# Kernel tuning notes

Hardware: AMD Instinct MI355X
Metric: run time of the kernel (lower is better)

Reference implementation:

```python
import jax, jax.numpy as jnp
import numpy as np

B, N, DIM = 128, 577, 1024
HEADS, DIM_HEAD = 16, 64
INNER = HEADS * DIM_HEAD  # must equal DIM per module's reshape constraint


def setup_inputs() -> dict:
    key = jax.random.key(0)
    ks = jax.random.split(key, 6)
    x = jax.random.normal(ks[0], (B, N, DIM), jnp.float32)
    W_proj = jax.random.normal(ks[1], (INNER, DIM), jnp.float32) * (DIM ** -0.5)
    step_x = jax.random.normal(ks[2], (HEADS, 1, 1), jnp.float32)
    step_rep = jax.random.normal(ks[3], (HEADS, 1, 1), jnp.float32)
    W_out = jax.random.normal(ks[4], (DIM, INNER), jnp.float32) * (INNER ** -0.5)
    b_out = jnp.zeros((DIM,), jnp.float32)
    return {"x": x, "W_proj": W_proj, "step_x": step_x,
            "step_rep": step_rep, "W_out": W_out, "b_out": b_out}


def _attention(q, k, v, scale):
    # q: (b,h,q,d), k/v: (b,h,k,d)
    attn = jax.nn.softmax(jnp.einsum('bhqd,bhkd->bhqk', q, k) * scale, axis=-1)
    out = jnp.einsum('bhqk,bhkd->bhqd', attn, v)
    return out, attn


def reference(x, W_proj, step_x, step_rep, W_out, b_out):
    b, n, c = x.shape
    heads = step_x.shape[0]
    dim_head = W_proj.shape[0] // heads
    scale = dim_head ** -0.5
    h = int(n ** 0.5)          # grid side; n = h*h + 1 (cls token dropped for pooling)
    s = h // 8                 # adaptive pool block size (h divisible by 8)

    w = x @ W_proj.T  # (b, n, inner)

    # AdaptiveAvgPool2d((8,8)) on (b,c,h,h) == 3x3 block mean here; token order row-major
    rep = w[:, :-1, :].reshape(b, 8, s, 8, s, c).mean(axis=(2, 4))  # (b,8,8,c)
    rep = rep.reshape(b, 64, heads, dim_head).transpose(0, 2, 1, 3)  # (b,h,64,d)
    wq = w.reshape(b, n, heads, dim_head).transpose(0, 2, 1, 3)      # (b,h,n,d)

    rep_delta, attn = _attention(rep, wq, wq, scale)  # attn: (b,h,64,n)
    rep = rep + step_rep * rep_delta

    x_delta, _ = _attention(rep, rep, rep, scale)     # (b,h,64,d)
    # attn.T @ x_delta : (b,h,n,64) @ (b,h,64,d) -> (b,h,n,d)
    x_delta = jnp.einsum('bhkn,bhkd->bhnd', attn, x_delta)
    x_delta = step_x * x_delta
    x_delta = x_delta.transpose(0, 2, 1, 3).reshape(b, n, heads * dim_head)
    return x_delta @ W_out.T + b_out
```

## Files before the change

### kernel.cpp

```cpp
#include <hip/hip_runtime.h>
#include <hip/hip_bf16.h>

typedef __hip_bfloat16 bf16;
typedef __attribute__((ext_vector_type(8))) short short8;
typedef __attribute__((ext_vector_type(4))) float floatx4;

#define N_TOK 577
#define DIM_ 1024

__device__ __forceinline__ float bf2f(bf16 v) { return __bfloat162float(v); }
__device__ __forceinline__ bf16 f2bf(float v) { return __float2bfloat16(v); }
__device__ __forceinline__ short f2bf_s(float f) {
  unsigned u = __builtin_bit_cast(unsigned, f);
  u = (u + 0x7FFFu + ((u >> 16) & 1u)) >> 16;
  return (short)u;
}

#define GLL16(g, l) __builtin_amdgcn_global_load_lds( \
    (const __attribute__((address_space(1))) void*)(g), \
    (__attribute__((address_space(3))) void*)(l), 16, 0, 0)

template <typename T>
__device__ __forceinline__ short8 ldfrag(const T* base) {
  if constexpr (sizeof(T) == 2) {
    return *(const short8*)base;
  } else {
    const floatx4* p = (const floatx4*)base;
    floatx4 a = p[0], b = p[1];
    short8 o;
    o[0] = f2bf_s(a[0]); o[1] = f2bf_s(a[1]); o[2] = f2bf_s(a[2]); o[3] = f2bf_s(a[3]);
    o[4] = f2bf_s(b[0]); o[5] = f2bf_s(b[1]); o[6] = f2bf_s(b[2]); o[7] = f2bf_s(b[3]);
    return o;
  }
}

__global__ __launch_bounds__(256) void cvt_f32_bf16_kernel(
    const float* __restrict__ in, bf16* __restrict__ out, long n8)
{
  const long stride = (long)gridDim.x * 256;
  for (long i = (long)blockIdx.x * 256 + threadIdx.x; i < n8; i += stride) {
    const floatx4* p = (const floatx4*)in + i * 2;
    floatx4 a = p[0], b = p[1];
    short8 o;
    o[0] = f2bf_s(a[0]); o[1] = f2bf_s(a[1]); o[2] = f2bf_s(a[2]); o[3] = f2bf_s(a[3]);
    o[4] = f2bf_s(b[0]); o[5] = f2bf_s(b[1]); o[6] = f2bf_s(b[2]); o[7] = f2bf_s(b[3]);
    ((short8*)out)[i] = o;
  }
}

template <typename TA, typename TB, typename TC>
__global__ __launch_bounds__(256) void gemm_bt_kernel(
    const TA* __restrict__ A, const TB* __restrict__ Bw,
    const float* __restrict__ bias, TC* __restrict__ C,
    int M, int N, int K)
{
  __shared__ TA As[128 * 32];
  __shared__ TB Bs[128 * 32];
  const int tid = threadIdx.x;
  const int wave = tid >> 6, lane = tid & 63;
  const int r = lane & 15, q = lane >> 4;
  const int m0 = blockIdx.y * 128, n0 = blockIdx.x * 128;
  const int wm = (wave >> 1) * 64, wn = (wave & 1) * 64;

  floatx4 acc[4][4];
#pragma unroll
  for (int i = 0; i < 4; ++i)
#pragma unroll
    for (int j = 0; j < 4; ++j) acc[i][j] = (floatx4){0.f, 0.f, 0.f, 0.f};

  const TA* Ab = A + (size_t)m0 * K;
  const TB* Bb = Bw + (size_t)n0 * K;
  const int srowA2 = wave * 32 + (lane >> 2), skkA2 = (lane & 3) * 8;
  const int srowA4 = wave * 32 + (lane >> 3), skkA4 = (lane & 7) * 4;

  for (int k0 = 0; k0 < K; k0 += 32) {
    if constexpr (sizeof(TA) == 2) {
      GLL16(Ab + (size_t)srowA2 * K + k0 + skkA2, As + wave * 1024);
      GLL16(Ab + (size_t)(srowA2 + 16) * K + k0 + skkA2, As + wave * 1024 + 512);
    } else {
      GLL16(Ab + (size_t)srowA4 * K + k0 + skkA4, As + wave * 1024);
      GLL16(Ab + (size_t)(srowA4 + 8) * K + k0 + skkA4, As + wave * 1024 + 256);
      GLL16(Ab + (size_t)(srowA4 + 16) * K + k0 + skkA4, As + wave * 1024 + 512);
      GLL16(Ab + (size_t)(srowA4 + 24) * K + k0 + skkA4, As + wave * 1024 + 768);
    }
    if constexpr (sizeof(TB) == 2) {
      GLL16(Bb + (size_t)srowA2 * K + k0 + skkA2, Bs + wave * 1024);
      GLL16(Bb + (size_t)(srowA2 + 16) * K + k0 + skkA2, Bs + wave * 1024 + 512);
    } else {
      GLL16(Bb + (size_t)srowA4 * K + k0 + skkA4, Bs + wave * 1024);
      GLL16(Bb + (size_t)(srowA4 + 8) * K + k0 + skkA4, Bs + wave * 1024 + 256);
      GLL16(Bb + (size_t)(srowA4 + 16) * K + k0 + skkA4, Bs + wave * 1024 + 512);
      GLL16(Bb + (size_t)(srowA4 + 24) * K + k0 + skkA4, Bs + wave * 1024 + 768);
    }
    __syncthreads();
    short8 af[4], bfr[4];
#pragma unroll
    for (int i = 0; i < 4; ++i)
      af[i] = ldfrag(As + (wm + i * 16 + r) * 32 + q * 8);
#pragma unroll
    for (int j = 0; j < 4; ++j)
      bfr[j] = ldfrag(Bs + (wn + j * 16 + r) * 32 + q * 8);
#pragma unroll
    for (int i = 0; i < 4; ++i)
#pragma unroll
      for (int j = 0; j < 4; ++j)
        acc[i][j] = __builtin_amdgcn_mfma_f32_16x16x32_bf16(af[i], bfr[j], acc[i][j], 0, 0, 0);
    __syncthreads();
  }

#pragma unroll
  for (int j = 0; j < 4; ++j) {
    const int col = n0 + wn + j * 16 + r;
    const float bv = bias ? bias[col] : 0.f;
#pragma unroll
    for (int i = 0; i < 4; ++i) {
      size_t base = (size_t)(m0 + wm + i * 16 + q * 4) * N + col;
#pragma unroll
      for (int t = 0; t < 4; ++t) {
        float v = acc[i][j][t] + bv;
        if constexpr (sizeof(TC) == 2) C[base + (size_t)t * N] = f2bf(v);
        else                           C[base + (size_t)t * N] = v;
      }
    }
  }
}

__global__ void pool_kernel(const bf16* __restrict__ w, bf16* __restrict__ repb)
{
  const int idx = blockIdx.x * 256 + threadIdx.x;
  const int d = idx & 63;
  const int p = (idx >> 6) & 63;
  const int h = (idx >> 12) & 15;
  const int b = idx >> 16;
  const int c = h * 64 + d;
  const int py = p >> 3, px = p & 7;
  const bf16* wb = w + (size_t)b * N_TOK * DIM_ + c;
  float s = 0.f;
#pragma unroll
  for (int dy = 0; dy < 3; ++dy)
#pragma unroll
    for (int dx = 0; dx < 3; ++dx) {
      int n = (py * 3 + dy) * 24 + px * 3 + dx;
      s += bf2f(wb[(size_t)n * DIM_]);
    }
  repb[idx] = f2bf(s * (1.f / 9.f));
}

__global__ __launch_bounds__(256) void attn1_kernel(
    const bf16* __restrict__ w, const bf16* __restrict__ rep_old,
    bf16* __restrict__ rep_new, float* __restrict__ mst,
    float* __restrict__ lst, const float* __restrict__ step_rep)
{
  __shared__ bf16 Qs[64 * 64];
  __shared__ bf16 Ks[32 * 64];
  __shared__ bf16 Ps[4][16 * 32];

  const int tid = threadIdx.x;
  const int wave = tid >> 6, lane = tid & 63;
  const int r = lane & 15, q = lane >> 4;
  const int bh = blockIdx.x;
  const int b = bh >> 4, h = bh & 15;
  const bf16* wbase = w + (size_t)b * N_TOK * DIM_ + h * 64;

  {
    const short8* src = (const short8*)(rep_old + (size_t)bh * 4096);
    short8* dst = (short8*)Qs;
    dst[tid] = src[tid];
    dst[tid + 256] = src[tid + 256];
  }
  __syncthreads();

  short8 qf[2];
#pragma unroll
  for (int t = 0; t < 2; ++t)
    qf[t] = *(const short8*)(Qs + (wave * 16 + r) * 64 + t * 32 + q * 8);

  const float scale = 0.125f;
  float mrow[4], lrow[4];
#pragma unroll
  for (int j = 0; j < 4; ++j) { mrow[j] = -1e30f; lrow[j] = 0.f; }

  for (int t0 = 0; t0 < 640; t0 += 32) {
    __syncthreads();
    {
      int key = t0 + (tid >> 3);
      int ck = (tid & 7) * 8;
      int kc = key < N_TOK ? key : N_TOK - 1;
      *(short8*)(Ks + (tid >> 3) * 64 + ck) =
          *(const short8*)(wbase + (size_t)kc * DIM_ + ck);
    }
    __syncthreads();
#pragma unroll
    for (int s = 0; s < 2; ++s) {
      floatx4 sf = (floatx4){0.f, 0.f, 0.f, 0.f};
#pragma unroll
      for (int t = 0; t < 2; ++t) {
        short8 kf = *(const short8*)(Ks + (s * 16 + r) * 64 + t * 32 + q * 8);
        sf = __builtin_amdgcn_mfma_f32_16x16x32_bf16(qf[t], kf, sf, 0, 0, 0);
      }
      const int key = t0 + s * 16 + r;
      const bool valid = key < N_TOK;
#pragma unroll
      for (int j = 0; j < 4; ++j) {
        float v = valid ? sf[j] * scale : -1e30f;
        float mn = fmaxf(mrow[j], v);
        lrow[j] = lrow[j] * __expf(mrow[j] - mn) + __expf(v - mn);
        mrow[j] = mn;
      }
    }
  }
#pragma unroll
  for (int off = 1; off < 16; off <<= 1) {
#pragma unroll
    for (int j = 0; j < 4; ++j) {
      float mo = __shfl_xor(mrow[j], off, 64);
      float lo = __shfl_xor(lrow[j], off, 64);
      float mn = fmaxf(mrow[j], mo);
      lrow[j] = lrow[j] * __expf(mrow[j] - mn) + lo * __expf(mo - mn);
      mrow[j] = mn;
    }
  }
  float rli[4];
#pragma unroll
  for (int j = 0; j < 4; ++j) rli[j] = 1.f / lrow[j];

  if (r == 0) {
#pragma unroll
    for (int j = 0; j < 4; ++j) {
      const int row = wave * 16 + q * 4 + j;
      mst[(size_t)bh * 64 + row] = mrow[j];
      lst[(size_t)bh * 64 + row] = rli[j];
    }
  }

  floatx4 oacc[4];
#pragma unroll
  for (int ds = 0; ds < 4; ++ds) oacc[ds] = (floatx4){0.f, 0.f, 0.f, 0.f};

  for (int t0 = 0; t0 < 640; t0 += 32) {
    __syncthreads();
    {
      int key = t0 + (tid >> 3);
      int ck = (tid & 7) * 8;
      int kc = key < N_TOK ? key : N_TOK - 1;
      *(short8*)(Ks + (tid >> 3) * 64 + ck) =
          *(const short8*)(wbase + (size_t)kc * DIM_ + ck);
    }
    __syncthreads();
#pragma unroll
    for (int s = 0; s < 2; ++s) {
      floatx4 sf = (floatx4){0.f, 0.f, 0.f, 0.f};
#pragma unroll
      for (int t = 0; t < 2; ++t) {
        short8 kf = *(const short8*)(Ks + (s * 16 + r) * 64 + t * 32 + q * 8);
        sf = __builtin_amdgcn_mfma_f32_16x16x32_bf16(qf[t], kf, sf, 0, 0, 0);
      }
      const int key = t0 + s * 16 + r;
      const bool valid = key < N_TOK;
#pragma unroll
      for (int j = 0; j < 4; ++j) {
        float pv = valid ? __expf(sf[j] * scale - mrow[j]) * rli[j] : 0.f;
        Ps[wave][(q * 4 + j) * 32 + s * 16 + r] = f2bf(pv);
      }
    }
    __syncthreads();
    short8 pa = *(const short8*)(Ps[wave] + r * 32 + q * 8);
#pragma unroll
    for (int ds = 0; ds < 4; ++ds) {
      short8 vf;
#pragma unroll
      for (int j = 0; j < 8; ++j)
        vf[j] = ((const short*)Ks)[(q * 8 + j) * 64 + ds * 16 + r];
      oacc[ds] = __builtin_amdgcn_mfma_f32_16x16x32_bf16(pa, vf, oacc[ds], 0, 0, 0);
    }
  }

  const float srep = step_rep[h];
#pragma unroll
  for (int ds = 0; ds < 4; ++ds)
#pragma unroll
    for (int j = 0; j < 4; ++j) {
      const int row = wave * 16 + q * 4 + j;
      const int d = ds * 16 + r;
      float old = bf2f(Qs[row * 64 + d]);
      rep_new[(size_t)bh * 4096 + row * 64 + d] = f2bf(old + srep * oacc[ds][j]);
    }
}

__global__ __launch_bounds__(256) void attn2_kernel(
    const bf16* repb, bf16* xd2)
{
  __shared__ bf16 Rs[64 * 64];
  __shared__ bf16 RsT[64 * 64];
  __shared__ bf16 Ps2[4][16 * 64];
  const int tid = threadIdx.x;
  const int wave = tid >> 6, lane = tid & 63;
  const int r = lane & 15, q = lane >> 4;
  const int bh = blockIdx.x;
  const bf16* rb = repb + (size_t)bh * 4096;
  {
    const short8* src = (const short8*)rb;
    short8 v0 = src[tid * 2];
    short8 v1 = src[tid * 2 + 1];
    ((short8*)Rs)[tid * 2] = v0;
    ((short8*)Rs)[tid * 2 + 1] = v1;
    int row = tid >> 2;
    int dbase = (tid & 3) * 16;
#pragma unroll
    for (int i = 0; i < 8; ++i) ((short*)RsT)[(dbase + i) * 64 + row] = v0[i];
#pragma unroll
    for (int i = 0; i < 8; ++i) ((short*)RsT)[(dbase + 8 + i) * 64 + row] = v1[i];
  }
  __syncthreads();

  short8 qf[2];
#pragma unroll
  for (int t = 0; t < 2; ++t)
    qf[t] = *(const short8*)(Rs + (wave * 16 + r) * 64 + t * 32 + q * 8);

  floatx4 sacc[4];
#pragma unroll
  for (int ns = 0; ns < 4; ++ns) {
    sacc[ns] = (floatx4){0.f, 0.f, 0.f, 0.f};
#pragma unroll
    for (int t = 0; t < 2; ++t) {
      short8 kf = *(const short8*)(Rs + (ns * 16 + r) * 64 + t * 32 + q * 8);
      sacc[ns] = __builtin_amdgcn_mfma_f32_16x16x32_bf16(qf[t], kf, sacc[ns], 0, 0, 0);
    }
  }
  const float scale = 0.125f;
#pragma unroll
  for (int j = 0; j < 4; ++j) {
    float m = sacc[0][j];
#pragma unroll
    for (int ns = 1; ns < 4; ++ns) m = fmaxf(m, sacc[ns][j]);
#pragma unroll
    for (int off = 1; off < 16; off <<= 1) m = fmaxf(m, __shfl_xor(m, off, 64));
    float l = 0.f;
#pragma unroll
    for (int ns = 0; ns < 4; ++ns) {
      float e = __expf((sacc[ns][j] - m) * scale);
      sacc[ns][j] = e;
      l += e;
    }
#pragma unroll
    for (int off = 1; off < 16; off <<= 1) l += __shfl_xor(l, off, 64);
    float inv = 1.f / l;
#pragma unroll
    for (int ns = 0; ns < 4; ++ns)
      Ps2[wave][(q * 4 + j) * 64 + ns * 16 + r] = f2bf(sacc[ns][j] * inv);
  }
  __syncthreads();

  short8 pa[2];
#pragma unroll
  for (int t = 0; t < 2; ++t)
    pa[t] = *(const short8*)(Ps2[wave] + r * 64 + t * 32 + q * 8);
  bf16* ob = xd2 + (size_t)bh * 4096;
#pragma unroll
  for (int ds = 0; ds < 4; ++ds) {
    floatx4 o = (floatx4){0.f, 0.f, 0.f, 0.f};
#pragma unroll
    for (int t = 0; t < 2; ++t) {
      short8 vf = *(const short8*)(RsT + (ds * 16 + r) * 64 + t * 32 + q * 8);
      o = __builtin_amdgcn_mfma_f32_16x16x32_bf16(pa[t], vf, o, 0, 0, 0);
    }
#pragma unroll
    for (int j = 0; j < 4; ++j)
      ob[(size_t)(wave * 16 + q * 4 + j) * 64 + ds * 16 + r] = f2bf(o[j]);
  }
}

__global__ __launch_bounds__(256) void applyattn_kernel(
    bf16* wx, const bf16* __restrict__ qold, const bf16* __restrict__ xd2,
    const float* __restrict__ mst, const float* __restrict__ lst,
    const float* __restrict__ step_x)
{
  __shared__ bf16 Qold[64 * 64];
  __shared__ bf16 X2s[64 * 64];
  __shared__ bf16 Kt[64 * 64];
  __shared__ bf16 Pt[64 * 64];
  __shared__ float mlds[64], llds[64];
  const int tid = threadIdx.x;
  const int wave = tid >> 6, lane = tid & 63;
  const int r = lane & 15, q = lane >> 4;
  const int bh = blockIdx.x;
  const int b = bh >> 4, h = bh & 15;
  bf16* wbase = wx + (size_t)b * N_TOK * DIM_ + h * 64;

  {
    const short8* s1 = (const short8*)(qold + (size_t)bh * 4096);
    const short8* s2 = (const short8*)(xd2 + (size_t)bh * 4096);
    ((short8*)Qold)[tid] = s1[tid];
    ((short8*)Qold)[tid + 256] = s1[tid + 256];
    ((short8*)X2s)[tid] = s2[tid];
    ((short8*)X2s)[tid + 256] = s2[tid + 256];
    if (tid < 64) {
      mlds[tid] = mst[(size_t)bh * 64 + tid];
      llds[tid] = lst[(size_t)bh * 64 + tid];
    }
  }
  __syncthreads();

  short8 aq[4][2];
#pragma unroll
  for (int kt = 0; kt < 4; ++kt)
#pragma unroll
    for (int t = 0; t < 2; ++t)
      aq[kt][t] = *(const short8*)(Qold + (kt * 16 + r) * 64 + t * 32 + q * 8);
  short8 bx[4][2];
#pragma unroll
  for (int ds = 0; ds < 4; ++ds)
#pragma unroll
    for (int t = 0; t < 2; ++t) {
      short8 v;
#pragma unroll
      for (int j = 0; j < 8; ++j)
        v[j] = ((const short*)X2s)[(t * 32 + q * 8 + j) * 64 + ds * 16 + r];
      bx[ds][t] = v;
    }
  float mh[4][4], lh[4][4];
#pragma unroll
  for (int kt = 0; kt < 4; ++kt)
#pragma unroll
    for (int j = 0; j < 4; ++j) {
      mh[kt][j] = mlds[kt * 16 + q * 4 + j];
      lh[kt][j] = llds[kt * 16 + q * 4 + j];
    }
  const float sx = step_x[h];
  const float scale = 0.125f;

  for (int n0 = 0; n0 < N_TOK; n0 += 64) {
    __syncthreads();
    {
      int row = tid >> 2, nb = (tid & 3) * 16;
      int nrow = n0 + row;
      if (nrow > N_TOK - 1) nrow = N_TOK - 1;
      *(short8*)(Kt + row * 64 + nb) =
          *(const short8*)(wbase + (size_t)nrow * DIM_ + nb);
      *(short8*)(Kt + row * 64 + nb + 8) =
          *(const short8*)(wbase + (size_t)nrow * DIM_ + nb + 8);
    }
    __syncthreads();
    short8 kb[2];
#pragma unroll
    for (int t = 0; t < 2; ++t)
      kb[t] = *(const short8*)(Kt + (wave * 16 + r) * 64 + t * 32 + q * 8);
#pragma unroll
    for (int kt = 0; kt < 4; ++kt) {
      floatx4 sf = (floatx4){0.f, 0.f, 0.f, 0.f};
#pragma unroll
      for (int t = 0; t < 2; ++t)
        sf = __builtin_amdgcn_mfma_f32_16x16x32_bf16(aq[kt][t], kb[t], sf, 0, 0, 0);
#pragma unroll
      for (int j = 0; j < 4; ++j) {
        float p = __expf(sf[j] * scale - mh[kt][j]) * lh[kt][j];
        Pt[(kt * 16 + q * 4 + j) * 64 + wave * 16 + r] = f2bf(p);
      }
    }
    __syncthreads();
    short8 pa[2];
#pragma unroll
    for (int t = 0; t < 2; ++t) {
      short8 v;
#pragma unroll
      for (int j = 0; j < 8; ++j)
        v[j] = ((const short*)Pt)[(t * 32 + q * 8 + j) * 64 + wave * 16 + r];
      pa[t] = v;
    }
#pragma unroll
    for (int ds = 0; ds < 4; ++ds) {
      floatx4 o = (floatx4){0.f, 0.f, 0.f, 0.f};
#pragma unroll
      for (int t = 0; t < 2; ++t)
        o = __builtin_amdgcn_mfma_f32_16x16x32_bf16(pa[t], bx[ds][t], o, 0, 0, 0);
#pragma unroll
      for (int j = 0; j < 4; ++j) {
        int n = n0 + wave * 16 + q * 4 + j;
        if (n < N_TOK)
          wbase[(size_t)n * DIM_ + ds * 16 + r] = f2bf(o[j] * sx);
      }
    }
  }
}

extern "C" void kernel_launch(void* const* d_in, const int* in_sizes, int n_in,
                              void* d_out, int out_size, void* d_ws, size_t ws_size,
                              hipStream_t stream)
{
  const float* x        = (const float*)d_in[0];
  const float* W_proj   = (const float*)d_in[1];
  const float* step_x   = (const float*)d_in[2];
  const float* step_rep = (const float*)d_in[3];
  const float* W_out    = (const float*)d_in[4];
  const float* b_out    = (const float*)d_in[5];
  float* out = (float*)d_out;

  char* ws = (char*)d_ws;
  bf16*  wbuf   = (bf16*)ws;
  bf16*  xb     = (bf16*)(ws + 151257088ULL);
  bf16*  repold = (bf16*)(ws + 151257088ULL);
  bf16*  repnew = (bf16*)(ws + 168034304ULL);
  float* mst    = (float*)(ws + 184811520ULL);
  float* lst    = (float*)(ws + 185335808ULL);
  bf16*  wprojb = (bf16*)(ws + 302514176ULL);
  bf16*  woutb  = (bf16*)(ws + 304611328ULL);

  const size_t WS_FALLBACK = 185860096ULL;
  const size_t WS_BF16     = 306708480ULL;
  if (ws_size < WS_FALLBACK) return;
  const bool use_bf16 = ws_size >= WS_BF16;

  const int M = 128 * N_TOK;

  if (use_bf16) {
    const long n8_x = (long)M * DIM_ / 8;
    const long n8_w = (long)DIM_ * DIM_ / 8;
    cvt_f32_bf16_kernel<<<4096, 256, 0, stream>>>(x, xb, n8_x);
    cvt_f32_bf16_kernel<<<512, 256, 0, stream>>>(W_proj, wprojb, n8_w);
    cvt_f32_bf16_kernel<<<512, 256, 0, stream>>>(W_out, woutb, n8_w);
    gemm_bt_kernel<bf16, bf16, bf16><<<dim3(8, 577), 256, 0, stream>>>(
        xb, wprojb, nullptr, wbuf, M, DIM_, DIM_);
  } else {
    gemm_bt_kernel<float, float, bf16><<<dim3(8, 577), 256, 0, stream>>>(
        x, W_proj, nullptr, wbuf, M, DIM_, DIM_);
  }

  pool_kernel<<<32768, 256, 0, stream>>>(wbuf, repold);
  attn1_kernel<<<2048, 256, 0, stream>>>(wbuf, repold, repnew, mst, lst, step_rep);
  attn2_kernel<<<2048, 256, 0, stream>>>(repnew, repnew);
  applyattn_kernel<<<2048, 256, 0, stream>>>(wbuf, repold, repnew, mst, lst, step_x);

  if (use_bf16) {
    gemm_bt_kernel<bf16, bf16, float><<<dim3(8, 577), 256, 0, stream>>>(
        wbuf, woutb, b_out, out, M, DIM_, DIM_);
  } else {
    gemm_bt_kernel<bf16, float, float><<<dim3(8, 577), 256, 0, stream>>>(
        wbuf, W_out, b_out, out, M, DIM_, DIM_);
  }
}
```

Before: 1.213 ms.

## Swizzle GEMM block order across XCDs and stage bf16 epilogue through LDS

Switches the GEMM launch to a 1D grid and remaps block ids so that consecutive blocks, which the hardware spreads round-robin over 8 XCDs, land on contiguous tiles for each XCD. This is meant to improve L2 reuse of A and B tiles. For bf16 outputs, the epilogue now writes accumulators into XOR-swizzled shared memory in two halves and then stores 16-byte vectors per row instead of scattered 2-byte stores. The extra barriers and shared-memory round trip add some cost, and the swizzle assumes the block count is divisible by 8.

```diff
diff --git a/kernel.cpp b/kernel.cpp
--- a/kernel.cpp
+++ b/kernel.cpp
@@ -54,12 +54,19 @@
     const float* __restrict__ bias, TC* __restrict__ C,
     int M, int N, int K)
 {
-  __shared__ TA As[128 * 32];
-  __shared__ TB Bs[128 * 32];
+  __shared__ __align__(16) char smem[(sizeof(TA) + sizeof(TB)) * 128 * 32];
+  TA* As = (TA*)smem;
+  TB* Bs = (TB*)(smem + sizeof(TA) * 128 * 32);
+
   const int tid = threadIdx.x;
   const int wave = tid >> 6, lane = tid & 63;
   const int r = lane & 15, q = lane >> 4;
-  const int m0 = blockIdx.y * 128, n0 = blockIdx.x * 128;
+
+  const int NT = N >> 7;
+  const int chunk = gridDim.x >> 3;
+  const int id = blockIdx.x;
+  const int swz = (id & 7) * chunk + (id >> 3);
+  const int n0 = (swz % NT) * 128, m0 = (swz / NT) * 128;
   const int wm = (wave >> 1) * 64, wn = (wave & 1) * 64;
 
   floatx4 acc[4][4];
@@ -108,18 +115,48 @@
     __syncthreads();
   }
 
-#pragma unroll
-  for (int j = 0; j < 4; ++j) {
-    const int col = n0 + wn + j * 16 + r;
-    const float bv = bias ? bias[col] : 0.f;
-#pragma unroll
-    for (int i = 0; i < 4; ++i) {
-      size_t base = (size_t)(m0 + wm + i * 16 + q * 4) * N + col;
-#pragma unroll
-      for (int t = 0; t < 4; ++t) {
-        float v = acc[i][j][t] + bv;
-        if constexpr (sizeof(TC) == 2) C[base + (size_t)t * N] = f2bf(v);
-        else                           C[base + (size_t)t * N] = v;
+  if constexpr (sizeof(TC) == 2) {
+    char* Cs = smem;
+    const int orow = tid >> 2;
+    const int ob0 = (tid & 3) * 64;
+#pragma unroll
+    for (int half = 0; half < 2; ++half) {
+      __syncthreads();
+      if ((wave >> 1) == half) {
+#pragma unroll
+        for (int j = 0; j < 4; ++j) {
+          const int colb = (wn + j * 16 + r) * 2;
+          const float bv = bias ? bias[n0 + wn + j * 16 + r] : 0.f;
+#pragma unroll
+          for (int i = 0; i < 4; ++i)
+#pragma unroll
+            for (int t = 0; t < 4; ++t) {
+              const int lrow = i * 16 + q * 4 + t;
+              *(bf16*)(Cs + lrow * 256 + (colb ^ ((lrow & 7) << 4))) =
+                  f2bf(acc[i][j][t] + bv);
+            }
+        }
+      }
+      __syncthreads();
+      const size_t grow = (size_t)(m0 + half * 64 + orow) * N + n0;
+#pragma unroll
+      for (int it = 0; it < 4; ++it) {
+        const int byte = ob0 + it * 16;
+        short8 v = *(const short8*)(Cs + orow * 256 + (byte ^ ((orow & 7) << 4)));
+        *(short8*)((bf16*)C + grow + (byte >> 1)) = v;
+      }
+    }
+  } else {
+#pragma unroll
+    for (int j = 0; j < 4; ++j) {
+      const int col = n0 + wn + j * 16 + r;
+      const float bv = bias ? bias[col] : 0.f;
+#pragma unroll
+      for (int i = 0; i < 4; ++i) {
+        size_t base = (size_t)(m0 + wm + i * 16 + q * 4) * N + col;
+#pragma unroll
+        for (int t = 0; t < 4; ++t)
+          C[base + (size_t)t * N] = acc[i][j][t] + bv;
       }
     }
   }
@@ -512,6 +549,7 @@
   const bool use_bf16 = ws_size >= WS_BF16;
 
   const int M = 128 * N_TOK;
+  const int GEMM_BLOCKS = (M / 128) * (DIM_ / 128);
 
   if (use_bf16) {
     const long n8_x = (long)M * DIM_ / 8;
@@ -519,10 +557,10 @@
     cvt_f32_bf16_kernel<<<4096, 256, 0, stream>>>(x, xb, n8_x);
     cvt_f32_bf16_kernel<<<512, 256, 0, stream>>>(W_proj, wprojb, n8_w);
     cvt_f32_bf16_kernel<<<512, 256, 0, stream>>>(W_out, woutb, n8_w);
-    gemm_bt_kernel<bf16, bf16, bf16><<<dim3(8, 577), 256, 0, stream>>>(
+    gemm_bt_kernel<bf16, bf16, bf16><<<GEMM_BLOCKS, 256, 0, stream>>>(
         xb, wprojb, nullptr, wbuf, M, DIM_, DIM_);
   } else {
-    gemm_bt_kernel<float, float, bf16><<<dim3(8, 577), 256, 0, stream>>>(
+    gemm_bt_kernel<float, float, bf16><<<GEMM_BLOCKS, 256, 0, stream>>>(
         x, W_proj, nullptr, wbuf, M, DIM_, DIM_);
   }
 
@@ -532,10 +570,10 @@
   applyattn_kernel<<<2048, 256, 0, stream>>>(wbuf, repold, repnew, mst, lst, step_x);
 
   if (use_bf16) {
-    gemm_bt_kernel<bf16, bf16, float><<<dim3(8, 577), 256, 0, stream>>>(
+    gemm_bt_kernel<bf16, bf16, float><<<GEMM_BLOCKS, 256, 0, stream>>>(
         wbuf, woutb, b_out, out, M, DIM_, DIM_);
   } else {
-    gemm_bt_kernel<bf16, float, float><<<dim3(8, 577), 256, 0, stream>>>(
+    gemm_bt_kernel<bf16, float, float><<<GEMM_BLOCKS, 256, 0, stream>>>(
         wbuf, W_out, b_out, out, M, DIM_, DIM_);
   }
 }
```

Result: slower. 1.271 ms (+4.8%).
